# Performance work log

Hardware: AMD Instinct MI355X
Metric: run time of the kernel (lower is better)

Reference implementation:

```python
import jax, jax.numpy as jnp
import numpy as np

EMB = 1024
HEADS = 16
HEAD_DIM = EMB // HEADS
B, L = 2, 2048


def setup_inputs() -> dict:
    key = jax.random.key(0)
    k1, k2, k3, k4 = jax.random.split(key, 4)
    x = jax.random.normal(k1, (B, L, EMB), dtype=jnp.float32)
    # nn.Linear(emb, 3*emb, bias=False): weight [3E, E]; apply as x @ W.T
    w_qkv = jax.random.normal(k2, (3 * EMB, EMB), dtype=jnp.float32) * (EMB ** -0.5)
    w_out = jax.random.normal(k3, (EMB, EMB), dtype=jnp.float32) * (EMB ** -0.5)
    b_out = jax.random.normal(k4, (EMB,), dtype=jnp.float32) * 0.01
    return {"x": x, "w_qkv": w_qkv, "w_out": w_out, "b_out": b_out}


def reference(x, w_qkv, w_out, b_out):
    b, n, e = x.shape
    scale = HEAD_DIM ** -0.5
    qkv = x @ w_qkv.T                       # [B, L, 3E]
    q, k, v = jnp.split(qkv, 3, axis=-1)
    def heads(t):
        return t.reshape(b, n, HEADS, HEAD_DIM).transpose(0, 2, 1, 3)  # [B,H,L,d]
    q, k, v = heads(q), heads(k), heads(v)
    dots = jnp.einsum('bhid,bhjd->bhij', q, k) * scale   # [B,H,L,L]
    attn = jax.nn.softmax(dots, axis=-1)
    out = jnp.einsum('bhij,bhjd->bhid', attn, v)         # [B,H,L,d]
    out = out.transpose(0, 2, 1, 3).reshape(b, n, e)      # [B,L,E]
    out = out @ w_out.T + b_out
    return out, attn
```

## Files before the change

kernel.cpp:

```cpp
#include <hip/hip_runtime.h>


typedef __attribute__((ext_vector_type(8))) short bf16x8;
typedef __attribute__((ext_vector_type(4))) float f32x4;

__device__ __forceinline__ unsigned short f2bf(float f) {
  unsigned int u = __float_as_uint(f);
  u += 0x7fffu + ((u >> 16) & 1u);
  return (unsigned short)(u >> 16);
}

__global__ __launch_bounds__(256) void conv_bf16(
    const float* __restrict__ X, const float* __restrict__ Wqkv, const float* __restrict__ Wout,
    unsigned short* __restrict__ xb, unsigned short* __restrict__ wqkvb,
    unsigned short* __restrict__ woutb) {
  size_t e0 = ((size_t)blockIdx.x * 256 + threadIdx.x) * 8;
  const float* src; unsigned short* dst; size_t off;
  if (e0 < 4194304)      { src = X;    dst = xb;    off = e0; }
  else if (e0 < 7340032) { src = Wqkv; dst = wqkvb; off = e0 - 4194304; }
  else                   { src = Wout; dst = woutb; off = e0 - 7340032; }
  float4 a = *(const float4*)(src + off);
  float4 c = *(const float4*)(src + off + 4);
  int4 o;
  o.x = f2bf(a.x) | ((unsigned int)f2bf(a.y) << 16);
  o.y = f2bf(a.z) | ((unsigned int)f2bf(a.w) << 16);
  o.z = f2bf(c.x) | ((unsigned int)f2bf(c.y) << 16);
  o.w = f2bf(c.z) | ((unsigned int)f2bf(c.w) << 16);
  *(int4*)(dst + off) = o;
}

__global__ __launch_bounds__(256) void gemm_qkv(
    const unsigned short* __restrict__ XB, const unsigned short* __restrict__ WB,
    unsigned short* __restrict__ qk_ws, unsigned short* __restrict__ vt_ws) {
  __shared__ unsigned short smem[2 * 128 * 72];
  unsigned short* a_lds = smem;
  unsigned short* b_lds = smem + 128 * 72;
  const int tid = threadIdx.x;
  const int lane = tid & 63;
  const int wid = tid >> 6;
  const int wm = wid >> 1, wn = wid & 1;
  const int m0 = blockIdx.x * 128;
  const int n0 = blockIdx.y * 128;

  f32x4 acc[4][4];
#pragma unroll
  for (int i = 0; i < 4; ++i)
#pragma unroll
    for (int j = 0; j < 4; ++j) acc[i][j] = (f32x4){0.f, 0.f, 0.f, 0.f};

  for (int kt = 0; kt < 16; ++kt) {
    const int k0 = kt * 64;
#pragma unroll
    for (int i = 0; i < 4; ++i) {
      int c = i * 256 + tid;
      int row = c >> 3, cc = (c & 7) << 3;
      *(int4*)&a_lds[row * 72 + cc] = *(const int4*)(XB + (size_t)(m0 + row) * 1024 + k0 + cc);
      *(int4*)&b_lds[row * 72 + cc] = *(const int4*)(WB + (size_t)(n0 + row) * 1024 + k0 + cc);
    }
    __syncthreads();
#pragma unroll
    for (int ks = 0; ks < 2; ++ks) {
      bf16x8 af[4], bfr[4];
#pragma unroll
      for (int f = 0; f < 4; ++f) {
        af[f]  = *(const bf16x8*)&a_lds[(wm * 64 + f * 16 + (lane & 15)) * 72 + ks * 32 + (lane >> 4) * 8];
        bfr[f] = *(const bf16x8*)&b_lds[(wn * 64 + f * 16 + (lane & 15)) * 72 + ks * 32 + (lane >> 4) * 8];
      }
#pragma unroll
      for (int fi = 0; fi < 4; ++fi)
#pragma unroll
        for (int fj = 0; fj < 4; ++fj)
          acc[fi][fj] = __builtin_amdgcn_mfma_f32_16x16x32_bf16(af[fi], bfr[fj], acc[fi][fj], 0, 0, 0);
    }
    __syncthreads();
  }

  if (n0 < 2048) {
#pragma unroll
    for (int fi = 0; fi < 4; ++fi)
#pragma unroll
      for (int fj = 0; fj < 4; ++fj) {
        int row = wm * 64 + fi * 16 + ((lane >> 4) << 2);
        int col = wn * 64 + fj * 16 + (lane & 15);
#pragma unroll
        for (int r = 0; r < 4; ++r) smem[(row + r) * 136 + col] = f2bf(acc[fi][fj][r]);
      }
    __syncthreads();
#pragma unroll
    for (int i = 0; i < 8; ++i) {
      int c = i * 256 + tid;
      int row = c >> 4, cc = c & 15;
      *(int4*)(qk_ws + (size_t)(m0 + row) * 2048 + n0 + cc * 8) = *(const int4*)&smem[row * 136 + cc * 8];
    }
  } else {
#pragma unroll
    for (int fi = 0; fi < 4; ++fi)
#pragma unroll
      for (int fj = 0; fj < 4; ++fj) {
        int colg = n0 - 2048 + wn * 64 + fj * 16 + (lane & 15);
        int tok = m0 + wm * 64 + fi * 16 + ((lane >> 4) << 2);
        int bb = tok >> 11, lt = tok & 2047;
        int bh = bb * 16 + (colg >> 6);
        int dd = colg & 63;
        unsigned int p0 = f2bf(acc[fi][fj][0]) | ((unsigned int)f2bf(acc[fi][fj][1]) << 16);
        unsigned int p1 = f2bf(acc[fi][fj][2]) | ((unsigned int)f2bf(acc[fi][fj][3]) << 16);
        *(uint2*)(vt_ws + (size_t)(bh * 64 + dd) * 2048 + lt) = make_uint2(p0, p1);
      }
  }
}

__global__ __launch_bounds__(256) void attn_merged(
    const unsigned short* __restrict__ qk_ws, const unsigned short* __restrict__ vt_ws,
    float* __restrict__ attn_out, unsigned short* __restrict__ ao_ws) {
  __shared__ unsigned short k_lds[2][64 * 72];
  __shared__ unsigned short v_lds[2][64 * 72];
  __shared__ unsigned short e_lds[32 * 72];
  __shared__ float ls_rs[32];

  const int tid = threadIdx.x;
  const int lane = tid & 63;
  const int w = tid >> 6;
  const int bh = blockIdx.y;
  const int b = bh >> 4;
  const int h = bh & 15;
  const int q0 = blockIdx.x * 32;

  const int srow = tid >> 3;
  const int scc = (tid & 7) << 3;
  const size_t kg = (size_t)(b * 2048) * 2048 + 1024 + (size_t)h * 64 + scc;
  const size_t vg = ((size_t)(bh * 64 + srow)) * 2048 + scc;

  bf16x8 qf[2][2];
#pragma unroll
  for (int fi = 0; fi < 2; ++fi)
#pragma unroll
    for (int ks = 0; ks < 2; ++ks) {
      int tok = q0 + fi * 16 + (lane & 15);
      int col = h * 64 + ks * 32 + (lane >> 4) * 8;
      qf[fi][ks] = *(const bf16x8*)(qk_ws + ((size_t)(b * 2048 + tok)) * 2048 + col);
    }

  if (tid < 32) ls_rs[tid] = 0.f;

  int4 ka, kb;
  ka = *(const int4*)(qk_ws + kg + (size_t)(srow) * 2048);
  kb = *(const int4*)(qk_ws + kg + (size_t)(32 + srow) * 2048);
  *(int4*)&k_lds[0][srow * 72 + scc] = ka;
  *(int4*)&k_lds[0][(32 + srow) * 72 + scc] = kb;
  ka = *(const int4*)(qk_ws + kg + (size_t)(64 + srow) * 2048);
  kb = *(const int4*)(qk_ws + kg + (size_t)(96 + srow) * 2048);
  __syncthreads();

  float ps[2][4] = {{0.f, 0.f, 0.f, 0.f}, {0.f, 0.f, 0.f, 0.f}};
  for (int jt = 0; jt < 32; ++jt) {
    const int cur = jt & 1;
    if (jt + 1 < 32) {
      *(int4*)&k_lds[cur ^ 1][srow * 72 + scc] = ka;
      *(int4*)&k_lds[cur ^ 1][(32 + srow) * 72 + scc] = kb;
    }
    if (jt + 2 < 32) {
      ka = *(const int4*)(qk_ws + kg + (size_t)((jt + 2) * 64 + srow) * 2048);
      kb = *(const int4*)(qk_ws + kg + (size_t)((jt + 2) * 64 + 32 + srow) * 2048);
    }
    bf16x8 kf0 = *(const bf16x8*)&k_lds[cur][(w * 16 + (lane & 15)) * 72 + (lane >> 4) * 8];
    bf16x8 kf1 = *(const bf16x8*)&k_lds[cur][(w * 16 + (lane & 15)) * 72 + 32 + (lane >> 4) * 8];
    f32x4 s0 = (f32x4){0.f, 0.f, 0.f, 0.f}, s1 = (f32x4){0.f, 0.f, 0.f, 0.f};
    s0 = __builtin_amdgcn_mfma_f32_16x16x32_bf16(qf[0][0], kf0, s0, 0, 0, 0);
    s0 = __builtin_amdgcn_mfma_f32_16x16x32_bf16(qf[0][1], kf1, s0, 0, 0, 0);
    s1 = __builtin_amdgcn_mfma_f32_16x16x32_bf16(qf[1][0], kf0, s1, 0, 0, 0);
    s1 = __builtin_amdgcn_mfma_f32_16x16x32_bf16(qf[1][1], kf1, s1, 0, 0, 0);
#pragma unroll
    for (int r = 0; r < 4; ++r) {
      ps[0][r] += __expf(s0[r] * 0.125f);
      ps[1][r] += __expf(s1[r] * 0.125f);
    }
    __syncthreads();
  }

#pragma unroll
  for (int fi = 0; fi < 2; ++fi)
#pragma unroll
    for (int r = 0; r < 4; ++r) {
      float v = ps[fi][r];
      v += __shfl_xor(v, 1);
      v += __shfl_xor(v, 2);
      v += __shfl_xor(v, 4);
      v += __shfl_xor(v, 8);
      if ((lane & 15) == 0) atomicAdd(&ls_rs[fi * 16 + ((lane >> 4) << 2) + r], v);
    }
  __syncthreads();
  float inv[2][4];
#pragma unroll
  for (int fi = 0; fi < 2; ++fi)
#pragma unroll
    for (int r = 0; r < 4; ++r) inv[fi][r] = 1.0f / ls_rs[fi * 16 + ((lane >> 4) << 2) + r];

  f32x4 pv0 = (f32x4){0.f, 0.f, 0.f, 0.f}, pv1 = (f32x4){0.f, 0.f, 0.f, 0.f};
  int4 va, vb;
  ka = *(const int4*)(qk_ws + kg + (size_t)(srow) * 2048);
  kb = *(const int4*)(qk_ws + kg + (size_t)(32 + srow) * 2048);
  va = *(const int4*)(vt_ws + vg);
  vb = *(const int4*)(vt_ws + vg + 65536);
  *(int4*)&k_lds[0][srow * 72 + scc] = ka;
  *(int4*)&k_lds[0][(32 + srow) * 72 + scc] = kb;
  *(int4*)&v_lds[0][srow * 72 + scc] = va;
  *(int4*)&v_lds[0][(32 + srow) * 72 + scc] = vb;
  ka = *(const int4*)(qk_ws + kg + (size_t)(64 + srow) * 2048);
  kb = *(const int4*)(qk_ws + kg + (size_t)(96 + srow) * 2048);
  va = *(const int4*)(vt_ws + vg + 64);
  vb = *(const int4*)(vt_ws + vg + 65536 + 64);
  __syncthreads();

  for (int jt = 0; jt < 32; ++jt) {
    const int cur = jt & 1;
    const int j0 = jt * 64;
    if (jt + 1 < 32) {
      *(int4*)&k_lds[cur ^ 1][srow * 72 + scc] = ka;
      *(int4*)&k_lds[cur ^ 1][(32 + srow) * 72 + scc] = kb;
      *(int4*)&v_lds[cur ^ 1][srow * 72 + scc] = va;
      *(int4*)&v_lds[cur ^ 1][(32 + srow) * 72 + scc] = vb;
    }
    if (jt + 2 < 32) {
      ka = *(const int4*)(qk_ws + kg + (size_t)((jt + 2) * 64 + srow) * 2048);
      kb = *(const int4*)(qk_ws + kg + (size_t)((jt + 2) * 64 + 32 + srow) * 2048);
      va = *(const int4*)(vt_ws + vg + (jt + 2) * 64);
      vb = *(const int4*)(vt_ws + vg + 65536 + (jt + 2) * 64);
    }
    bf16x8 kf0 = *(const bf16x8*)&k_lds[cur][(w * 16 + (lane & 15)) * 72 + (lane >> 4) * 8];
    bf16x8 kf1 = *(const bf16x8*)&k_lds[cur][(w * 16 + (lane & 15)) * 72 + 32 + (lane >> 4) * 8];
    f32x4 s0 = (f32x4){0.f, 0.f, 0.f, 0.f}, s1 = (f32x4){0.f, 0.f, 0.f, 0.f};
    s0 = __builtin_amdgcn_mfma_f32_16x16x32_bf16(qf[0][0], kf0, s0, 0, 0, 0);
    s0 = __builtin_amdgcn_mfma_f32_16x16x32_bf16(qf[0][1], kf1, s0, 0, 0, 0);
    s1 = __builtin_amdgcn_mfma_f32_16x16x32_bf16(qf[1][0], kf0, s1, 0, 0, 0);
    s1 = __builtin_amdgcn_mfma_f32_16x16x32_bf16(qf[1][1], kf1, s1, 0, 0, 0);
    {
      int col = w * 16 + (lane & 15);
      int row0 = (lane >> 4) << 2;
#pragma unroll
      for (int r = 0; r < 4; ++r) {
        e_lds[(row0 + r) * 72 + col]      = f2bf(__expf(s0[r] * 0.125f) * inv[0][r]);
        e_lds[(16 + row0 + r) * 72 + col] = f2bf(__expf(s1[r] * 0.125f) * inv[1][r]);
      }
    }
    __syncthreads();
    {
      int row = tid >> 3;
      int c0 = (tid & 7) << 3;
      int4 raw = *(const int4*)&e_lds[row * 72 + c0];
      f32x4 o0, o1;
      o0.x = __uint_as_float(((unsigned int)raw.x) << 16);
      o0.y = __uint_as_float(((unsigned int)raw.x) & 0xffff0000u);
      o0.z = __uint_as_float(((unsigned int)raw.y) << 16);
      o0.w = __uint_as_float(((unsigned int)raw.y) & 0xffff0000u);
      o1.x = __uint_as_float(((unsigned int)raw.z) << 16);
      o1.y = __uint_as_float(((unsigned int)raw.z) & 0xffff0000u);
      o1.z = __uint_as_float(((unsigned int)raw.w) << 16);
      o1.w = __uint_as_float(((unsigned int)raw.w) & 0xffff0000u);
      size_t ab = ((size_t)bh * 2048 + q0 + row) * 2048 + j0 + c0;
      __builtin_nontemporal_store(o0, (f32x4*)(attn_out + ab));
      __builtin_nontemporal_store(o1, (f32x4*)(attn_out + ab + 4));
    }
#pragma unroll
    for (int ks = 0; ks < 2; ++ks) {
      bf16x8 vf  = *(const bf16x8*)&v_lds[cur][(w * 16 + (lane & 15)) * 72 + ks * 32 + (lane >> 4) * 8];
      bf16x8 ef0 = *(const bf16x8*)&e_lds[((lane & 15)) * 72 + ks * 32 + (lane >> 4) * 8];
      bf16x8 ef1 = *(const bf16x8*)&e_lds[(16 + (lane & 15)) * 72 + ks * 32 + (lane >> 4) * 8];
      pv0 = __builtin_amdgcn_mfma_f32_16x16x32_bf16(vf, ef0, pv0, 0, 0, 0);
      pv1 = __builtin_amdgcn_mfma_f32_16x16x32_bf16(vf, ef1, pv1, 0, 0, 0);
    }
    __syncthreads();
  }

#pragma unroll
  for (int mf = 0; mf < 2; ++mf) {
    f32x4 pv = mf ? pv1 : pv0;
    int tok = q0 + mf * 16 + (lane & 15);
    int d = w * 16 + ((lane >> 4) << 2);
    unsigned int p0 = f2bf(pv[0]) | ((unsigned int)f2bf(pv[1]) << 16);
    unsigned int p1 = f2bf(pv[2]) | ((unsigned int)f2bf(pv[3]) << 16);
    *(uint2*)(ao_ws + ((size_t)(b * 2048 + tok)) * 1024 + h * 64 + d) = make_uint2(p0, p1);
  }
}

__global__ __launch_bounds__(256) void gemm_out(
    const unsigned short* __restrict__ AO, const unsigned short* __restrict__ WB,
    const float* __restrict__ Bias, float* __restrict__ OUT) {
  __shared__ unsigned short smem[2 * 128 * 72];
  unsigned short* a_lds = smem;
  unsigned short* b_lds = smem + 128 * 72;
  const int tid = threadIdx.x;
  const int lane = tid & 63;
  const int wid = tid >> 6;
  const int wm = wid >> 1, wn = wid & 1;
  const int m0 = blockIdx.x * 128, n0 = blockIdx.y * 128;

  f32x4 acc[4][4];
#pragma unroll
  for (int i = 0; i < 4; ++i)
#pragma unroll
    for (int j = 0; j < 4; ++j) acc[i][j] = (f32x4){0.f, 0.f, 0.f, 0.f};

  for (int kt = 0; kt < 16; ++kt) {
    const int k0 = kt * 64;
#pragma unroll
    for (int i = 0; i < 4; ++i) {
      int c = i * 256 + tid;
      int row = c >> 3, cc = (c & 7) << 3;
      *(int4*)&a_lds[row * 72 + cc] = *(const int4*)(AO + (size_t)(m0 + row) * 1024 + k0 + cc);
      *(int4*)&b_lds[row * 72 + cc] = *(const int4*)(WB + (size_t)(n0 + row) * 1024 + k0 + cc);
    }
    __syncthreads();
#pragma unroll
    for (int ks = 0; ks < 2; ++ks) {
      bf16x8 af[4], bfr[4];
#pragma unroll
      for (int f = 0; f < 4; ++f) {
        af[f]  = *(const bf16x8*)&a_lds[(wm * 64 + f * 16 + (lane & 15)) * 72 + ks * 32 + (lane >> 4) * 8];
        bfr[f] = *(const bf16x8*)&b_lds[(wn * 64 + f * 16 + (lane & 15)) * 72 + ks * 32 + (lane >> 4) * 8];
      }
#pragma unroll
      for (int fi = 0; fi < 4; ++fi)
#pragma unroll
        for (int fj = 0; fj < 4; ++fj)
          acc[fi][fj] = __builtin_amdgcn_mfma_f32_16x16x32_bf16(af[fi], bfr[fj], acc[fi][fj], 0, 0, 0);
    }
    __syncthreads();
  }

  float* ftile = (float*)smem;
#pragma unroll
  for (int half = 0; half < 2; ++half) {
    if (wm == half) {
#pragma unroll
      for (int fi = 0; fi < 4; ++fi)
#pragma unroll
        for (int fj = 0; fj < 4; ++fj) {
          int row = fi * 16 + ((lane >> 4) << 2);
          int col = wn * 64 + fj * 16 + (lane & 15);
#pragma unroll
          for (int r = 0; r < 4; ++r) ftile[(row + r) * 136 + col] = acc[fi][fj][r];
        }
    }
    __syncthreads();
#pragma unroll
    for (int i = 0; i < 8; ++i) {
      int c = i * 256 + tid;
      int row = c >> 5, cc = c & 31;
      float4 v = *(const float4*)&ftile[row * 136 + cc * 4];
      float4 bb = *(const float4*)(Bias + n0 + cc * 4);
      v.x += bb.x; v.y += bb.y; v.z += bb.z; v.w += bb.w;
      *(float4*)(OUT + (size_t)(m0 + half * 64 + row) * 1024 + n0 + cc * 4) = v;
    }
    __syncthreads();
  }
}

extern "C" void kernel_launch(void* const* d_in, const int* in_sizes, int n_in,
                              void* d_out, int out_size, void* d_ws, size_t ws_size,
                              hipStream_t stream) {
  const float* x     = (const float*)d_in[0];
  const float* w_qkv = (const float*)d_in[1];
  const float* w_out = (const float*)d_in[2];
  const float* b_out = (const float*)d_in[3];

  float* out      = (float*)d_out;
  float* attn_out = out + (size_t)4096 * 1024;

  unsigned short* qk_ws = (unsigned short*)d_ws;
  unsigned short* vt_ws = qk_ws + (size_t)4096 * 2048;
  unsigned short* ao_ws = vt_ws + (size_t)32 * 64 * 2048;
  unsigned short* xb    = ao_ws + (size_t)4096 * 1024;
  unsigned short* wqkvb = xb + (size_t)4096 * 1024;
  unsigned short* woutb = wqkvb + (size_t)3072 * 1024;

  conv_bf16<<<4096, 256, 0, stream>>>(x, w_qkv, w_out, xb, wqkvb, woutb);
  gemm_qkv<<<dim3(32, 24), 256, 0, stream>>>(xb, wqkvb, qk_ws, vt_ws);
  attn_merged<<<dim3(64, 32), 256, 0, stream>>>(qk_ws, vt_ws, attn_out, ao_ws);
  gemm_out<<<dim3(32, 8), 256, 0, stream>>>(ao_ws, woutb, b_out, out);
}
```

Before: 702.3 us.

## Enlarge attention query tile to 64 and load K/V fragments directly into registers

The attention kernel now processes 64 queries per block instead of 32, halving the grid and K/V reloads per query. K and V^T fragments are read straight from global memory into MFMA operand registers with one-step prefetch, dropping the K/V LDS staging and the per-iteration barrier in the row-sum pass. The exp tile is double-buffered in LDS, and softmax normalization moves to the fp32 attention store and the final PV output. This trades LDS traffic and syncs for more register pressure, fewer blocks, and uncoalesced global fragment loads. The probabilities fed to the PV MFMA are now bf16 unnormalized exps, which changes rounding slightly.

```diff
diff --git a/kernel.cpp b/kernel.cpp
--- a/kernel.cpp
+++ b/kernel.cpp
@@ -109,76 +109,65 @@
   }
 }
 
-__global__ __launch_bounds__(256) void attn_merged(
+__global__ __launch_bounds__(256) void attn_fused(
     const unsigned short* __restrict__ qk_ws, const unsigned short* __restrict__ vt_ws,
     float* __restrict__ attn_out, unsigned short* __restrict__ ao_ws) {
-  __shared__ unsigned short k_lds[2][64 * 72];
-  __shared__ unsigned short v_lds[2][64 * 72];
-  __shared__ unsigned short e_lds[32 * 72];
-  __shared__ float ls_rs[32];
+  __shared__ unsigned short e_lds[2][64 * 72];
+  __shared__ float ls_rs[64];
+  __shared__ float ls_inv[64];
 
   const int tid = threadIdx.x;
   const int lane = tid & 63;
   const int w = tid >> 6;
+  const int l15 = lane & 15;
+  const int l4 = lane >> 4;
   const int bh = blockIdx.y;
   const int b = bh >> 4;
   const int h = bh & 15;
-  const int q0 = blockIdx.x * 32;
-
-  const int srow = tid >> 3;
-  const int scc = (tid & 7) << 3;
-  const size_t kg = (size_t)(b * 2048) * 2048 + 1024 + (size_t)h * 64 + scc;
-  const size_t vg = ((size_t)(bh * 64 + srow)) * 2048 + scc;
-
-  bf16x8 qf[2][2];
-#pragma unroll
-  for (int fi = 0; fi < 2; ++fi)
-#pragma unroll
-    for (int ks = 0; ks < 2; ++ks) {
-      int tok = q0 + fi * 16 + (lane & 15);
-      int col = h * 64 + ks * 32 + (lane >> 4) * 8;
-      qf[fi][ks] = *(const bf16x8*)(qk_ws + ((size_t)(b * 2048 + tok)) * 2048 + col);
-    }
-
-  if (tid < 32) ls_rs[tid] = 0.f;
-
-  int4 ka, kb;
-  ka = *(const int4*)(qk_ws + kg + (size_t)(srow) * 2048);
-  kb = *(const int4*)(qk_ws + kg + (size_t)(32 + srow) * 2048);
-  *(int4*)&k_lds[0][srow * 72 + scc] = ka;
-  *(int4*)&k_lds[0][(32 + srow) * 72 + scc] = kb;
-  ka = *(const int4*)(qk_ws + kg + (size_t)(64 + srow) * 2048);
-  kb = *(const int4*)(qk_ws + kg + (size_t)(96 + srow) * 2048);
+  const int q0 = blockIdx.x * 64;
+
+  const unsigned short* kp = qk_ws + ((size_t)(b * 2048 + w * 16 + l15)) * 2048 + 1024 + h * 64 + l4 * 8;
+  const size_t KJ = (size_t)64 * 2048;
+  const unsigned short* vp = vt_ws + ((size_t)(bh * 64 + w * 16 + l15)) * 2048 + l4 * 8;
+
+  bf16x8 qf[4][2];
+#pragma unroll
+  for (int fi = 0; fi < 4; ++fi)
+#pragma unroll
+    for (int ks = 0; ks < 2; ++ks)
+      qf[fi][ks] = *(const bf16x8*)(qk_ws + ((size_t)(b * 2048 + q0 + fi * 16 + l15)) * 2048 + h * 64 + ks * 32 + l4 * 8);
+
+  float ps[4][4];
+#pragma unroll
+  for (int fi = 0; fi < 4; ++fi)
+#pragma unroll
+    for (int r = 0; r < 4; ++r) ps[fi][r] = 0.f;
+
+  bf16x8 kn0 = *(const bf16x8*)(kp);
+  bf16x8 kn1 = *(const bf16x8*)(kp + 32);
+  for (int jt = 0; jt < 32; ++jt) {
+    bf16x8 kc0 = kn0, kc1 = kn1;
+    if (jt + 1 < 32) {
+      kn0 = *(const bf16x8*)(kp + (jt + 1) * KJ);
+      kn1 = *(const bf16x8*)(kp + (jt + 1) * KJ + 32);
+    }
+    f32x4 s[4];
+#pragma unroll
+    for (int fi = 0; fi < 4; ++fi) {
+      s[fi] = (f32x4){0.f, 0.f, 0.f, 0.f};
+      s[fi] = __builtin_amdgcn_mfma_f32_16x16x32_bf16(qf[fi][0], kc0, s[fi], 0, 0, 0);
+      s[fi] = __builtin_amdgcn_mfma_f32_16x16x32_bf16(qf[fi][1], kc1, s[fi], 0, 0, 0);
+    }
+#pragma unroll
+    for (int fi = 0; fi < 4; ++fi)
+#pragma unroll
+      for (int r = 0; r < 4; ++r) ps[fi][r] += __expf(s[fi][r] * 0.125f);
+  }
+
+  if (tid < 64) ls_rs[tid] = 0.f;
   __syncthreads();
-
-  float ps[2][4] = {{0.f, 0.f, 0.f, 0.f}, {0.f, 0.f, 0.f, 0.f}};
-  for (int jt = 0; jt < 32; ++jt) {
-    const int cur = jt & 1;
-    if (jt + 1 < 32) {
-      *(int4*)&k_lds[cur ^ 1][srow * 72 + scc] = ka;
-      *(int4*)&k_lds[cur ^ 1][(32 + srow) * 72 + scc] = kb;
-    }
-    if (jt + 2 < 32) {
-      ka = *(const int4*)(qk_ws + kg + (size_t)((jt + 2) * 64 + srow) * 2048);
-      kb = *(const int4*)(qk_ws + kg + (size_t)((jt + 2) * 64 + 32 + srow) * 2048);
-    }
-    bf16x8 kf0 = *(const bf16x8*)&k_lds[cur][(w * 16 + (lane & 15)) * 72 + (lane >> 4) * 8];
-    bf16x8 kf1 = *(const bf16x8*)&k_lds[cur][(w * 16 + (lane & 15)) * 72 + 32 + (lane >> 4) * 8];
-    f32x4 s0 = (f32x4){0.f, 0.f, 0.f, 0.f}, s1 = (f32x4){0.f, 0.f, 0.f, 0.f};
-    s0 = __builtin_amdgcn_mfma_f32_16x16x32_bf16(qf[0][0], kf0, s0, 0, 0, 0);
-    s0 = __builtin_amdgcn_mfma_f32_16x16x32_bf16(qf[0][1], kf1, s0, 0, 0, 0);
-    s1 = __builtin_amdgcn_mfma_f32_16x16x32_bf16(qf[1][0], kf0, s1, 0, 0, 0);
-    s1 = __builtin_amdgcn_mfma_f32_16x16x32_bf16(qf[1][1], kf1, s1, 0, 0, 0);
-#pragma unroll
-    for (int r = 0; r < 4; ++r) {
-      ps[0][r] += __expf(s0[r] * 0.125f);
-      ps[1][r] += __expf(s1[r] * 0.125f);
-    }
-    __syncthreads();
-  }
-
-#pragma unroll
-  for (int fi = 0; fi < 2; ++fi)
+#pragma unroll
+  for (int fi = 0; fi < 4; ++fi)
 #pragma unroll
     for (int r = 0; r < 4; ++r) {
       float v = ps[fi][r];
@@ -186,98 +175,97 @@
       v += __shfl_xor(v, 2);
       v += __shfl_xor(v, 4);
       v += __shfl_xor(v, 8);
-      if ((lane & 15) == 0) atomicAdd(&ls_rs[fi * 16 + ((lane >> 4) << 2) + r], v);
+      if (l15 == 0) atomicAdd(&ls_rs[fi * 16 + l4 * 4 + r], v);
     }
   __syncthreads();
-  float inv[2][4];
-#pragma unroll
-  for (int fi = 0; fi < 2; ++fi)
-#pragma unroll
-    for (int r = 0; r < 4; ++r) inv[fi][r] = 1.0f / ls_rs[fi * 16 + ((lane >> 4) << 2) + r];
-
-  f32x4 pv0 = (f32x4){0.f, 0.f, 0.f, 0.f}, pv1 = (f32x4){0.f, 0.f, 0.f, 0.f};
-  int4 va, vb;
-  ka = *(const int4*)(qk_ws + kg + (size_t)(srow) * 2048);
-  kb = *(const int4*)(qk_ws + kg + (size_t)(32 + srow) * 2048);
-  va = *(const int4*)(vt_ws + vg);
-  vb = *(const int4*)(vt_ws + vg + 65536);
-  *(int4*)&k_lds[0][srow * 72 + scc] = ka;
-  *(int4*)&k_lds[0][(32 + srow) * 72 + scc] = kb;
-  *(int4*)&v_lds[0][srow * 72 + scc] = va;
-  *(int4*)&v_lds[0][(32 + srow) * 72 + scc] = vb;
-  ka = *(const int4*)(qk_ws + kg + (size_t)(64 + srow) * 2048);
-  kb = *(const int4*)(qk_ws + kg + (size_t)(96 + srow) * 2048);
-  va = *(const int4*)(vt_ws + vg + 64);
-  vb = *(const int4*)(vt_ws + vg + 65536 + 64);
+  if (tid < 64) ls_inv[tid] = 1.0f / ls_rs[tid];
   __syncthreads();
-
+  float inv_col[4];
+#pragma unroll
+  for (int mf = 0; mf < 4; ++mf) inv_col[mf] = ls_inv[mf * 16 + l15];
+
+  f32x4 pv[4];
+#pragma unroll
+  for (int mf = 0; mf < 4; ++mf) pv[mf] = (f32x4){0.f, 0.f, 0.f, 0.f};
+
+  const int srow = tid >> 2;
+  const int sc0 = (tid & 3) << 4;
+  const float siv = ls_inv[srow];
+
+  kn0 = *(const bf16x8*)(kp);
+  kn1 = *(const bf16x8*)(kp + 32);
+  bf16x8 vn0 = *(const bf16x8*)(vp);
+  bf16x8 vn1 = *(const bf16x8*)(vp + 32);
   for (int jt = 0; jt < 32; ++jt) {
     const int cur = jt & 1;
-    const int j0 = jt * 64;
+    bf16x8 kc0 = kn0, kc1 = kn1, vc0 = vn0, vc1 = vn1;
     if (jt + 1 < 32) {
-      *(int4*)&k_lds[cur ^ 1][srow * 72 + scc] = ka;
-      *(int4*)&k_lds[cur ^ 1][(32 + srow) * 72 + scc] = kb;
-      *(int4*)&v_lds[cur ^ 1][srow * 72 + scc] = va;
-      *(int4*)&v_lds[cur ^ 1][(32 + srow) * 72 + scc] = vb;
-    }
-    if (jt + 2 < 32) {
-      ka = *(const int4*)(qk_ws + kg + (size_t)((jt + 2) * 64 + srow) * 2048);
-      kb = *(const int4*)(qk_ws + kg + (size_t)((jt + 2) * 64 + 32 + srow) * 2048);
-      va = *(const int4*)(vt_ws + vg + (jt + 2) * 64);
-      vb = *(const int4*)(vt_ws + vg + 65536 + (jt + 2) * 64);
-    }
-    bf16x8 kf0 = *(const bf16x8*)&k_lds[cur][(w * 16 + (lane & 15)) * 72 + (lane >> 4) * 8];
-    bf16x8 kf1 = *(const bf16x8*)&k_lds[cur][(w * 16 + (lane & 15)) * 72 + 32 + (lane >> 4) * 8];
-    f32x4 s0 = (f32x4){0.f, 0.f, 0.f, 0.f}, s1 = (f32x4){0.f, 0.f, 0.f, 0.f};
-    s0 = __builtin_amdgcn_mfma_f32_16x16x32_bf16(qf[0][0], kf0, s0, 0, 0, 0);
-    s0 = __builtin_amdgcn_mfma_f32_16x16x32_bf16(qf[0][1], kf1, s0, 0, 0, 0);
-    s1 = __builtin_amdgcn_mfma_f32_16x16x32_bf16(qf[1][0], kf0, s1, 0, 0, 0);
-    s1 = __builtin_amdgcn_mfma_f32_16x16x32_bf16(qf[1][1], kf1, s1, 0, 0, 0);
+      kn0 = *(const bf16x8*)(kp + (jt + 1) * KJ);
+      kn1 = *(const bf16x8*)(kp + (jt + 1) * KJ + 32);
+      vn0 = *(const bf16x8*)(vp + (jt + 1) * 64);
+      vn1 = *(const bf16x8*)(vp + (jt + 1) * 64 + 32);
+    }
+    f32x4 s[4];
+#pragma unroll
+    for (int fi = 0; fi < 4; ++fi) {
+      s[fi] = (f32x4){0.f, 0.f, 0.f, 0.f};
+      s[fi] = __builtin_amdgcn_mfma_f32_16x16x32_bf16(qf[fi][0], kc0, s[fi], 0, 0, 0);
+      s[fi] = __builtin_amdgcn_mfma_f32_16x16x32_bf16(qf[fi][1], kc1, s[fi], 0, 0, 0);
+    }
+#pragma unroll
+    for (int fi = 0; fi < 4; ++fi) {
+      int row0 = fi * 16 + l4 * 4;
+      int col = w * 16 + l15;
+#pragma unroll
+      for (int r = 0; r < 4; ++r)
+        e_lds[cur][(row0 + r) * 72 + col] = f2bf(__expf(s[fi][r] * 0.125f));
+    }
+    __syncthreads();
     {
-      int col = w * 16 + (lane & 15);
-      int row0 = (lane >> 4) << 2;
-#pragma unroll
-      for (int r = 0; r < 4; ++r) {
-        e_lds[(row0 + r) * 72 + col]      = f2bf(__expf(s0[r] * 0.125f) * inv[0][r]);
-        e_lds[(16 + row0 + r) * 72 + col] = f2bf(__expf(s1[r] * 0.125f) * inv[1][r]);
-      }
-    }
-    __syncthreads();
-    {
-      int row = tid >> 3;
-      int c0 = (tid & 7) << 3;
-      int4 raw = *(const int4*)&e_lds[row * 72 + c0];
-      f32x4 o0, o1;
-      o0.x = __uint_as_float(((unsigned int)raw.x) << 16);
-      o0.y = __uint_as_float(((unsigned int)raw.x) & 0xffff0000u);
-      o0.z = __uint_as_float(((unsigned int)raw.y) << 16);
-      o0.w = __uint_as_float(((unsigned int)raw.y) & 0xffff0000u);
-      o1.x = __uint_as_float(((unsigned int)raw.z) << 16);
-      o1.y = __uint_as_float(((unsigned int)raw.z) & 0xffff0000u);
-      o1.z = __uint_as_float(((unsigned int)raw.w) << 16);
-      o1.w = __uint_as_float(((unsigned int)raw.w) & 0xffff0000u);
-      size_t ab = ((size_t)bh * 2048 + q0 + row) * 2048 + j0 + c0;
-      __builtin_nontemporal_store(o0, (f32x4*)(attn_out + ab));
-      __builtin_nontemporal_store(o1, (f32x4*)(attn_out + ab + 4));
+      int4 raw0 = *(const int4*)&e_lds[cur][srow * 72 + sc0];
+      int4 raw1 = *(const int4*)&e_lds[cur][srow * 72 + sc0 + 8];
+      size_t ab = ((size_t)bh * 2048 + q0 + srow) * 2048 + jt * 64 + sc0;
+      f32x4 o;
+      o.x = __uint_as_float(((unsigned int)raw0.x) << 16) * siv;
+      o.y = __uint_as_float(((unsigned int)raw0.x) & 0xffff0000u) * siv;
+      o.z = __uint_as_float(((unsigned int)raw0.y) << 16) * siv;
+      o.w = __uint_as_float(((unsigned int)raw0.y) & 0xffff0000u) * siv;
+      __builtin_nontemporal_store(o, (f32x4*)(attn_out + ab));
+      o.x = __uint_as_float(((unsigned int)raw0.z) << 16) * siv;
+      o.y = __uint_as_float(((unsigned int)raw0.z) & 0xffff0000u) * siv;
+      o.z = __uint_as_float(((unsigned int)raw0.w) << 16) * siv;
+      o.w = __uint_as_float(((unsigned int)raw0.w) & 0xffff0000u) * siv;
+      __builtin_nontemporal_store(o, (f32x4*)(attn_out + ab + 4));
+      o.x = __uint_as_float(((unsigned int)raw1.x) << 16) * siv;
+      o.y = __uint_as_float(((unsigned int)raw1.x) & 0xffff0000u) * siv;
+      o.z = __uint_as_float(((unsigned int)raw1.y) << 16) * siv;
+      o.w = __uint_as_float(((unsigned int)raw1.y) & 0xffff0000u) * siv;
+      __builtin_nontemporal_store(o, (f32x4*)(attn_out + ab + 8));
+      o.x = __uint_as_float(((unsigned int)raw1.z) << 16) * siv;
+      o.y = __uint_as_float(((unsigned int)raw1.z) & 0xffff0000u) * siv;
+      o.z = __uint_as_float(((unsigned int)raw1.w) << 16) * siv;
+      o.w = __uint_as_float(((unsigned int)raw1.w) & 0xffff0000u) * siv;
+      __builtin_nontemporal_store(o, (f32x4*)(attn_out + ab + 12));
     }
 #pragma unroll
     for (int ks = 0; ks < 2; ++ks) {
-      bf16x8 vf  = *(const bf16x8*)&v_lds[cur][(w * 16 + (lane & 15)) * 72 + ks * 32 + (lane >> 4) * 8];
-      bf16x8 ef0 = *(const bf16x8*)&e_lds[((lane & 15)) * 72 + ks * 32 + (lane >> 4) * 8];
-      bf16x8 ef1 = *(const bf16x8*)&e_lds[(16 + (lane & 15)) * 72 + ks * 32 + (lane >> 4) * 8];
-      pv0 = __builtin_amdgcn_mfma_f32_16x16x32_bf16(vf, ef0, pv0, 0, 0, 0);
-      pv1 = __builtin_amdgcn_mfma_f32_16x16x32_bf16(vf, ef1, pv1, 0, 0, 0);
-    }
-    __syncthreads();
-  }
-
-#pragma unroll
-  for (int mf = 0; mf < 2; ++mf) {
-    f32x4 pv = mf ? pv1 : pv0;
-    int tok = q0 + mf * 16 + (lane & 15);
-    int d = w * 16 + ((lane >> 4) << 2);
-    unsigned int p0 = f2bf(pv[0]) | ((unsigned int)f2bf(pv[1]) << 16);
-    unsigned int p1 = f2bf(pv[2]) | ((unsigned int)f2bf(pv[3]) << 16);
+      bf16x8 vfk = ks ? vc1 : vc0;
+#pragma unroll
+      for (int mf = 0; mf < 4; ++mf) {
+        bf16x8 ef = *(const bf16x8*)&e_lds[cur][(mf * 16 + l15) * 72 + ks * 32 + l4 * 8];
+        pv[mf] = __builtin_amdgcn_mfma_f32_16x16x32_bf16(vfk, ef, pv[mf], 0, 0, 0);
+      }
+    }
+    __syncthreads();
+  }
+
+#pragma unroll
+  for (int mf = 0; mf < 4; ++mf) {
+    int tok = q0 + mf * 16 + l15;
+    int d = w * 16 + l4 * 4;
+    float iv = inv_col[mf];
+    unsigned int p0 = f2bf(pv[mf][0] * iv) | ((unsigned int)f2bf(pv[mf][1] * iv) << 16);
+    unsigned int p1 = f2bf(pv[mf][2] * iv) | ((unsigned int)f2bf(pv[mf][3] * iv) << 16);
     *(uint2*)(ao_ws + ((size_t)(b * 2048 + tok)) * 1024 + h * 64 + d) = make_uint2(p0, p1);
   }
 }
@@ -375,6 +363,6 @@
 
   conv_bf16<<<4096, 256, 0, stream>>>(x, w_qkv, w_out, xb, wqkvb, woutb);
   gemm_qkv<<<dim3(32, 24), 256, 0, stream>>>(xb, wqkvb, qk_ws, vt_ws);
-  attn_merged<<<dim3(64, 32), 256, 0, stream>>>(qk_ws, vt_ws, attn_out, ao_ws);
+  attn_fused<<<dim3(32, 32), 256, 0, stream>>>(qk_ws, vt_ws, attn_out, ao_ws);
   gemm_out<<<dim3(32, 8), 256, 0, stream>>>(ao_ws, woutb, b_out, out);
 }
```

Measured after the change: 1.262 ms. 79.7% more time.
